# Performance work log

Hardware: AMD Instinct MI355X
Metric: run time of the kernel (lower is better)

The kernel has to match this reference:

```python
import jax, jax.numpy as jnp
import numpy as np

A0 = 0.529177249
SIGMA = jnp.array([0.5515909, 1.8886297, 1.3225029, 1.2316629,
                   2.1884933, 1.7750372, 1.3677907, 1.3820058], dtype=jnp.float32)


def celu(x):
    return jax.nn.celu(x, alpha=0.1)


def setup_inputs() -> dict:
    key = jax.random.key(0)
    ks = jax.random.split(key, 24)
    N, n, L, E = 512, 64, 384, 8
    H1, H2, H3 = 160, 128, 96
    s = 0.05
    f32 = jnp.float32
    return {
        "species": jax.random.randint(ks[0], (N, n), 0, E, dtype=jnp.int32),
        "coordinates": 3.0 * jax.random.normal(ks[1], (N, n, 3), dtype=f32),
        "net_charge": jax.random.normal(ks[2], (N,), dtype=f32),
        "aev": jax.random.normal(ks[3], (N, n, L), dtype=f32),
        "chi_W1": s * jax.random.normal(ks[4], (L, H1), dtype=f32),
        "chi_b1": s * jax.random.normal(ks[5], (H1,), dtype=f32),
        "chi_W2": s * jax.random.normal(ks[6], (H1, H2), dtype=f32),
        "chi_b2": s * jax.random.normal(ks[7], (H2,), dtype=f32),
        "chi_W3": s * jax.random.normal(ks[8], (H2, H3), dtype=f32),
        "chi_b3": s * jax.random.normal(ks[9], (H3,), dtype=f32),
        "chi_W4": s * jax.random.normal(ks[10], (H3, 1), dtype=f32),
        "chi_b4": s * jax.random.normal(ks[11], (1,), dtype=f32),
        "W1": s * jax.random.normal(ks[12], (E, L + 2, H1), dtype=f32),
        "b1": s * jax.random.normal(ks[13], (E, H1), dtype=f32),
        "W2": s * jax.random.normal(ks[14], (E, H1, H2), dtype=f32),
        "b2": s * jax.random.normal(ks[15], (E, H2), dtype=f32),
        "W3": s * jax.random.normal(ks[16], (E, H2, H3), dtype=f32),
        "b3": s * jax.random.normal(ks[17], (E, H3), dtype=f32),
        "W4": s * jax.random.normal(ks[18], (E, H3), dtype=f32),
        "b4": s * jax.random.normal(ks[19], (E,), dtype=f32),
    }


def _forward(species, coordinates, net_charge, aev,
             chi_W1, chi_b1, chi_W2, chi_b2, chi_W3, chi_b3, chi_W4, chi_b4,
             W1, b1, W2, b2, W3, b3, W4, b4):
    N, n = species.shape
    aev_flat = aev.reshape(N * n, -1)                       # (A, L)

    # nonzero_batch_dmat: distances in atomic units, eps avoids div-by-zero
    diff = coordinates[:, None, :, :] - coordinates[:, :, None, :]
    dist = jnp.sqrt(jnp.sum(diff * diff, -1) + 1e-16) / A0   # (N, n, n)

    pad = (species != -1).astype(aev.dtype)                  # (N, n)
    pair_mask = pad[:, None, :] * pad[:, :, None]            # (N, n, n)
    num_atoms = pad.sum(axis=1)                              # (N,)
    valid = (species.reshape(-1) != -1)                      # (A,)

    # chi_net: 4-layer MLP (CELU 0.1) + Softplus, masked to valid atoms
    h = celu(aev_flat @ chi_W1 + chi_b1)
    h = celu(h @ chi_W2 + chi_b2)
    h = celu(h @ chi_W3 + chi_b3)
    chi = jax.nn.softplus(h @ chi_W4 + chi_b4)[:, 0]
    chi = jnp.where(valid, chi, 0.0).reshape(N, n)

    chi_sum = chi.sum(axis=-1)
    k_net = 1.0 + jnp.abs(net_charge) / chi_sum
    chi_mean = chi_sum / num_atoms
    k_p = jnp.where(net_charge > 0, k_net, 1.0)
    k_n = jnp.where(net_charge < 0, k_net, 1.0)
    q = (-k_n[:, None] * chi + (k_p * chi_mean)[:, None]) * pad  # (N, n)

    # ESPerf: pairwise erf-screened Coulomb potential
    sig = SIGMA[jnp.clip(species, 0)]                        # (N, n)
    sig_sqsum = sig[:, None, :] ** 2 + sig[:, :, None] ** 2
    sig_sqsum = jnp.maximum(sig_sqsum, 1e-8)
    j_ij = jax.scipy.special.erf(dist / jnp.sqrt(2.0 * sig_sqsum)) / dist
    diag_mask = 1.0 - jnp.eye(n, dtype=dist.dtype)
    esp = (q[:, :, None] * j_ij * pair_mask * diag_mask[None]).sum(axis=-2)  # (N, n)
    coulomb_energy = 0.5 * (q * esp).sum(axis=-1)            # (N,)

    # species-routed expert MLPs over [aev | charge | esp] features
    feat = jnp.concatenate(
        [aev_flat, q.reshape(-1, 1), esp.reshape(-1, 1)], axis=1)  # (A, L+2)
    h1 = celu(jnp.einsum('ad,edh->aeh', feat, W1) + b1)      # (A, E, H1)
    h2 = celu(jnp.einsum('aeh,ehk->aek', h1, W2) + b2)       # (A, E, H2)
    h3 = celu(jnp.einsum('aek,ekm->aem', h2, W3) + b3)       # (A, E, H3)
    out_all = jnp.einsum('aem,em->ae', h3, W4) + b4          # (A, E)

    sp = jnp.clip(species.reshape(-1), 0)
    out = jnp.take_along_axis(out_all, sp[:, None], axis=1)[:, 0]
    out = jnp.where(valid, out, 0.0).reshape(N, n)
    mol_energy = out.sum(axis=1)
    return species, mol_energy + coulomb_energy, q


def reference(species, coordinates, net_charge, aev,
              chi_W1, chi_b1, chi_W2, chi_b2, chi_W3, chi_b3, chi_W4, chi_b4,
              W1, b1, W2, b2, W3, b3, W4, b4):
    return _forward(species, coordinates, net_charge, aev,
                    chi_W1, chi_b1, chi_W2, chi_b2, chi_W3, chi_b3, chi_W4, chi_b4,
                    W1, b1, W2, b2, W3, b3, W4, b4)
```

## Files before the change

kernel.cpp:

```cpp
#include <hip/hip_runtime.h>
#include <math.h>

#define A0_INV (1.0f/0.529177249f)

typedef __bf16 bf16x8 __attribute__((ext_vector_type(8)));
typedef __bf16 bf16x4 __attribute__((ext_vector_type(4)));
typedef float  f32x4  __attribute__((ext_vector_type(4)));

__device__ __constant__ float c_SIGMA[8] = {
    0.5515909f, 1.8886297f, 1.3225029f, 1.2316629f,
    2.1884933f, 1.7750372f, 1.3677907f, 1.3820058f};

__device__ __forceinline__ float celu01(float x) {
    return x > 0.0f ? x : 0.1f * (__expf(x * 10.0f) - 1.0f);
}
__device__ __forceinline__ float softplusf_(float x) {
    return fmaxf(x, 0.0f) + log1pf(__expf(-fabsf(x)));
}

__device__ __forceinline__ void pack_one(int idx, const float* __restrict__ W,
                                         __bf16* __restrict__ Bp,
                                         int K, int OUT, int NT, int KT)
{
    int lane = idx & 63;
    int rest = idx >> 6;
    int kt = rest % KT; rest /= KT;
    int nt = rest % NT;
    int e  = rest / NT;
    int col = nt * 16 + (lane & 15);
    int k0  = kt * 32 + (lane >> 4) * 8;
    bf16x8 o;
#pragma unroll
    for (int j = 0; j < 8; ++j) {
        int k = k0 + j;
        float v = (k < K) ? W[((long)e * K + k) * OUT + col] : 0.0f;
        o[j] = (__bf16)v;
    }
    *((bf16x8*)Bp + idx) = o;
}

__global__ __launch_bounds__(256) void pack_all_kernel(
    const float* __restrict__ cW1, const float* __restrict__ cW2, const float* __restrict__ cW3,
    const float* __restrict__ W1,  const float* __restrict__ W2,  const float* __restrict__ W3,
    __bf16* bp_c1, __bf16* bp_c2, __bf16* bp_c3,
    __bf16* bp_e1, __bf16* bp_e2, __bf16* bp_e3)
{
    int idx = blockIdx.x * 256 + threadIdx.x;
    if      (idx <   7680) pack_one(idx,          cW1, bp_c1, 384, 160, 10, 12);
    else if (idx <  10240) pack_one(idx - 7680,   cW2, bp_c2, 160, 128,  8,  5);
    else if (idx <  11776) pack_one(idx - 10240,  cW3, bp_c3, 128,  96,  6,  4);
    else if (idx <  78336) pack_one(idx - 11776,  W1,  bp_e1, 386, 160, 10, 13);
    else if (idx <  98816) pack_one(idx - 78336,  W2,  bp_e2, 160, 128,  8,  5);
    else if (idx < 111104) pack_one(idx - 98816,  W3,  bp_e3, 128,  96,  6,  4);
}

template<int NT, int KT, int INS, int OUTS, bool CELU>
__device__ __forceinline__ void mlp_layer8(const __bf16* sIn, const bf16x8* __restrict__ Bp,
                                           const float* __restrict__ bias, __bf16* sOut, int tid)
{
    const int lane = tid & 63;
    const int wid  = tid >> 6;
    const int mw   = wid >> 2;
    const int nw   = wid & 3;
    const int r16  = lane & 15;
    const int g    = lane >> 4;
    constexpr int NJ = (NT + 3) / 4;
    f32x4 acc[2][NJ];
#pragma unroll
    for (int mi = 0; mi < 2; ++mi)
#pragma unroll
        for (int j = 0; j < NJ; ++j)
            acc[mi][j] = (f32x4){0.f, 0.f, 0.f, 0.f};

    bf16x8 bcur[NJ], bnxt[NJ];
#pragma unroll
    for (int j = 0; j < NJ; ++j) {
        const int nt = nw + 4 * j;
        if (nt < NT) bcur[j] = Bp[(nt * KT) * 64 + lane];
    }
    for (int kt = 0; kt < KT; ++kt) {
        bf16x8 a[2];
#pragma unroll
        for (int mi = 0; mi < 2; ++mi)
            a[mi] = *(const bf16x8*)(sIn + ((mw * 2 + mi) * 16 + r16) * INS + kt * 32 + g * 8);
        if (kt + 1 < KT) {
#pragma unroll
            for (int j = 0; j < NJ; ++j) {
                const int nt = nw + 4 * j;
                if (nt < NT) bnxt[j] = Bp[(nt * KT + kt + 1) * 64 + lane];
            }
        }
#pragma unroll
        for (int j = 0; j < NJ; ++j) {
            const int nt = nw + 4 * j;
            if (nt < NT) {
#pragma unroll
                for (int mi = 0; mi < 2; ++mi)
                    acc[mi][j] = __builtin_amdgcn_mfma_f32_16x16x32_bf16(a[mi], bcur[j], acc[mi][j], 0, 0, 0);
            }
        }
#pragma unroll
        for (int j = 0; j < NJ; ++j) bcur[j] = bnxt[j];
    }
#pragma unroll
    for (int j = 0; j < NJ; ++j) {
        const int nt = nw + 4 * j;
        if (nt < NT) {
            const float bb = bias[nt * 16 + r16];
#pragma unroll
            for (int mi = 0; mi < 2; ++mi)
#pragma unroll
                for (int r = 0; r < 4; ++r) {
                    float v = acc[mi][j][r] + bb;
                    if (CELU) v = celu01(v);
                    sOut[((mw * 2 + mi) * 16 + g * 4 + r) * OUTS + nt * 16 + r16] = (__bf16)v;
                }
        }
    }
}

__device__ __forceinline__ float l4_dot(const __bf16* __restrict__ h,
                                        const float* __restrict__ w4)
{
    float acc = 0.f;
#pragma unroll
    for (int u8 = 0; u8 < 12; ++u8) {
        bf16x8 hv = *(const bf16x8*)(h + u8 * 8);
        float4 wa = *(const float4*)(w4 + u8 * 8);
        float4 wb = *(const float4*)(w4 + u8 * 8 + 4);
        acc = fmaf((float)hv[0], wa.x, acc);
        acc = fmaf((float)hv[1], wa.y, acc);
        acc = fmaf((float)hv[2], wa.z, acc);
        acc = fmaf((float)hv[3], wa.w, acc);
        acc = fmaf((float)hv[4], wb.x, acc);
        acc = fmaf((float)hv[5], wb.y, acc);
        acc = fmaf((float)hv[6], wb.z, acc);
        acc = fmaf((float)hv[7], wb.w, acc);
    }
    return acc;
}

__global__ __launch_bounds__(512) void chi_mfma_kernel(
    const float* __restrict__ aev, const int* __restrict__ species,
    const __bf16* __restrict__ bp1, const __bf16* __restrict__ bp2, const __bf16* __restrict__ bp3,
    const float* __restrict__ b1, const float* __restrict__ b2, const float* __restrict__ b3,
    const float* __restrict__ W4, const float* __restrict__ b4,
    float* __restrict__ chi_out, __bf16* __restrict__ aev16,
    int* __restrict__ blockCounts, int* __restrict__ rank)
{
    __shared__ __align__(16) unsigned char smem[50176 + 21504];
    __bf16* sFeat = (__bf16*)smem;
    __bf16* sAct1 = (__bf16*)(smem + 50176);
    __bf16* sAct2 = (__bf16*)smem;
    __bf16* sAct3 = (__bf16*)(smem + 17408);
    const int t = threadIdx.x;
    const long base = (long)blockIdx.x * 64;

    if (aev16) {
        for (int i = t; i < 64 * 96; i += 512) {
            int row = i / 96, c4 = (i - row * 96) * 4;
            float4 v = *(const float4*)(aev + (base + row) * 384 + c4);
            bf16x4 o = {(__bf16)v.x, (__bf16)v.y, (__bf16)v.z, (__bf16)v.w};
            *(bf16x4*)(sFeat + row * 392 + c4) = o;
            *(bf16x4*)(aev16 + (base + row) * 384 + c4) = o;
        }
    } else {
        for (int i = t; i < 64 * 96; i += 512) {
            int row = i / 96, c4 = (i - row * 96) * 4;
            float4 v = *(const float4*)(aev + (base + row) * 384 + c4);
            bf16x4 o = {(__bf16)v.x, (__bf16)v.y, (__bf16)v.z, (__bf16)v.w};
            *(bf16x4*)(sFeat + row * 392 + c4) = o;
        }
    }
    __syncthreads();
    mlp_layer8<10, 12, 392, 168, true>(sFeat, (const bf16x8*)bp1, b1, sAct1, t);
    __syncthreads();
    mlp_layer8<8, 5, 168, 136, true>(sAct1, (const bf16x8*)bp2, b2, sAct2, t);
    __syncthreads();
    mlp_layer8<6, 4, 136, 104, true>(sAct2, (const bf16x8*)bp3, b3, sAct3, t);
    __syncthreads();
    if (t < 64) {
        float acc = l4_dot(sAct3 + t * 104, W4);
        float chiv = softplusf_(acc + b4[0]);
        long atom = base + t;
        int s = species[atom];
        if (s == -1) chiv = 0.f;
        chi_out[atom] = chiv;
        unsigned long long mym = 0;
#pragma unroll
        for (int e = 0; e < 8; ++e) {
            unsigned long long bm = __ballot(s == e);
            if (t == e) blockCounts[blockIdx.x * 8 + e] = (int)__popcll(bm);
            if (s == e) mym = bm;
        }
        if (s >= 0) rank[atom] = (int)__popcll(mym & ((1ull << t) - 1ull));
    }
}

__global__ __launch_bounds__(256) void mol_kernel(
    const int* __restrict__ species, const float* __restrict__ coords,
    const float* __restrict__ netq, const float* __restrict__ chi,
    float* __restrict__ qv, float* __restrict__ esp, float* __restrict__ coul,
    float* __restrict__ o_species, float* __restrict__ o_q)
{
    const int m = blockIdx.x, t = threadIdx.x;
    const int j = t & 63, q4 = t >> 6;
    const int atom = m * 64 + j;
    __shared__ float sx[64], sy[64], sz[64], sq[64], ss2[64];
    __shared__ float sEsp[4][64];

    int s = species[atom];
    float pad = (s != -1) ? 1.0f : 0.0f;
    float chij = chi[atom];

    float cs = chij, na = pad;
#pragma unroll
    for (int o = 32; o > 0; o >>= 1) {
        cs += __shfl_xor(cs, o);
        na += __shfl_xor(na, o);
    }
    float qc = netq[m];
    float k_net = 1.0f + fabsf(qc) / cs;
    float chi_mean = cs / na;
    float k_p = (qc > 0.0f) ? k_net : 1.0f;
    float k_n = (qc < 0.0f) ? k_net : 1.0f;
    float qj = (-k_n * chij + k_p * chi_mean) * pad;

    float sg = c_SIGMA[s < 0 ? 0 : s];
    float x = coords[atom * 3 + 0], y = coords[atom * 3 + 1], z = coords[atom * 3 + 2];
    if (q4 == 0) { sx[j] = x; sy[j] = y; sz[j] = z; sq[j] = qj; ss2[j] = sg * sg; }
    __syncthreads();

    float s2j = sg * sg;
    float ej = 0.0f;
#pragma unroll
    for (int k = 0; k < 16; ++k) {
        int i = q4 * 16 + k;
        if (i == j) continue;
        float dx = sx[i] - x, dy = sy[i] - y, dz = sz[i] - z;
        float d = sqrtf(dx * dx + dy * dy + dz * dz + 1e-16f) * A0_INV;
        float ssum = fmaxf(ss2[i] + s2j, 1e-8f);
        float jij = erff(d * rsqrtf(2.0f * ssum)) / d;
        ej = fmaf(sq[i], jij, ej);
    }
    sEsp[q4][j] = ej;
    __syncthreads();
    if (q4 == 0) {
        float e = (sEsp[0][j] + sEsp[1][j]) + (sEsp[2][j] + sEsp[3][j]);
        e *= pad;
        float ce = qj * e;
#pragma unroll
        for (int o = 32; o > 0; o >>= 1) ce += __shfl_xor(ce, o);
        if (j == 0) coul[m] = 0.5f * ce;
        qv[atom] = qj;
        esp[atom] = e;
        o_species[atom] = (float)s;
        o_q[atom] = qj;
    }
}

__global__ void bucket_scan_kernel(int* __restrict__ blockCounts,
                                   int* __restrict__ counts, int* __restrict__ offs,
                                   int* __restrict__ workItems, int* __restrict__ workCount,
                                   int nb)
{
    __shared__ int segSum[8][8];
    __shared__ int tot[8];
    const int tid = threadIdx.x;
    const int seg = tid >> 3, e = tid & 7;
    const int per = (nb + 7) / 8;
    const int b0 = seg * per, b1 = min(b0 + per, nb);
    int run = 0;
    for (int b = b0; b < b1; ++b) run += blockCounts[b * 8 + e];
    segSum[seg][e] = run;
    __syncthreads();
    if (tid < 8) {
        int r = 0;
        for (int s2 = 0; s2 < 8; ++s2) { int c = segSum[s2][tid]; segSum[s2][tid] = r; r += c; }
        tot[tid] = r;
    }
    __syncthreads();
    int runp = segSum[seg][e];
    for (int b = b0; b < b1; ++b) {
        int c = blockCounts[b * 8 + e];
        blockCounts[b * 8 + e] = runp;
        runp += c;
    }
    if (tid == 0) {
        int o = 0;
        for (int i = 0; i < 8; ++i) { offs[i] = o; counts[i] = tot[i]; o += tot[i]; }
        offs[8] = o;
    }
    if (tid < 8) {
        int pos = 0;
        for (int i = 0; i < tid; ++i) pos += (tot[i] + 63) >> 6;
        int nt_e = (tot[tid] + 63) >> 6;
        for (int k = 0; k < nt_e; ++k) workItems[pos + k] = (tid << 20) | (k * 64);
        if (tid == 7) workCount[0] = pos + nt_e;
    }
}

__global__ __launch_bounds__(256) void bucket_fill_kernel(
    const int* __restrict__ species, const int* __restrict__ blockCounts,
    const int* __restrict__ offs, const int* __restrict__ rank,
    int* __restrict__ bidx, float* __restrict__ outat, int A)
{
    int a = blockIdx.x * 256 + threadIdx.x;
    if (a < A) {
        outat[a] = 0.0f;
        int s = species[a];
        if (s >= 0)
            bidx[offs[s] + blockCounts[(a >> 6) * 8 + s] + rank[a]] = a;
    }
}

__global__ __launch_bounds__(512) void expert_mfma_kernel(
    const float* __restrict__ aev, const __bf16* __restrict__ aev16,
    const float* __restrict__ qv, const float* __restrict__ esp,
    const __bf16* __restrict__ bp1, const __bf16* __restrict__ bp2, const __bf16* __restrict__ bp3,
    const float* __restrict__ b1, const float* __restrict__ b2, const float* __restrict__ b3,
    const float* __restrict__ W4, const float* __restrict__ b4,
    const int* __restrict__ counts, const int* __restrict__ offs, const int* __restrict__ bidx,
    const int* __restrict__ workItems, const int* __restrict__ workCount,
    float* __restrict__ outat)
{
    const int bid = blockIdx.x;
    if (bid >= workCount[0]) return;
    const int wi = workItems[bid];
    const int e = wi >> 20;
    const int start = wi & 0xFFFFF;
    const int cnt = counts[e];

    __shared__ __align__(16) unsigned char smem[54272 + 21504];
    __shared__ int said[64];
    __bf16* sFeat = (__bf16*)smem;
    __bf16* sAct1 = (__bf16*)(smem + 54272);
    __bf16* sAct2 = (__bf16*)smem;
    __bf16* sAct3 = (__bf16*)(smem + 17408);
    const int t = threadIdx.x;

    if (t < 64) said[t] = (start + t < cnt) ? bidx[offs[e] + start + t] : -1;
    __syncthreads();

    if (aev16) {
        for (int i = t; i < 64 * 48; i += 512) {
            int row = i / 48, c = (i - row * 48) * 8;
            int atom = said[row];
            bf16x8 v = {(__bf16)0.f, (__bf16)0.f, (__bf16)0.f, (__bf16)0.f,
                        (__bf16)0.f, (__bf16)0.f, (__bf16)0.f, (__bf16)0.f};
            if (atom >= 0) v = *(const bf16x8*)(aev16 + (long)atom * 384 + c);
            *(bf16x8*)(sFeat + row * 424 + c) = v;
        }
    } else {
        for (int i = t; i < 64 * 96; i += 512) {
            int row = i / 96, c4 = (i - row * 96) * 4;
            int atom = said[row];
            bf16x4 o = {(__bf16)0.f, (__bf16)0.f, (__bf16)0.f, (__bf16)0.f};
            if (atom >= 0) {
                float4 v = *(const float4*)(aev + (long)atom * 384 + c4);
                o[0] = (__bf16)v.x; o[1] = (__bf16)v.y;
                o[2] = (__bf16)v.z; o[3] = (__bf16)v.w;
            }
            *(bf16x4*)(sFeat + row * 424 + c4) = o;
        }
    }
    if (t < 64) {
        int atom = said[t];
        float a0 = 0.f, a1 = 0.f;
        if (atom >= 0) { a0 = qv[atom]; a1 = esp[atom]; }
        sFeat[t * 424 + 384] = (__bf16)a0;
        sFeat[t * 424 + 385] = (__bf16)a1;
        for (int c = 386; c < 416; ++c) sFeat[t * 424 + c] = (__bf16)0.f;
    }
    __syncthreads();
    mlp_layer8<10, 13, 424, 168, true>(sFeat, (const bf16x8*)bp1 + (size_t)e * 10 * 13 * 64,
                                       b1 + e * 160, sAct1, t);
    __syncthreads();
    mlp_layer8<8, 5, 168, 136, true>(sAct1, (const bf16x8*)bp2 + (size_t)e * 8 * 5 * 64,
                                     b2 + e * 128, sAct2, t);
    __syncthreads();
    mlp_layer8<6, 4, 136, 104, true>(sAct2, (const bf16x8*)bp3 + (size_t)e * 6 * 4 * 64,
                                     b3 + e * 96, sAct3, t);
    __syncthreads();
    if (t < 64) {
        int atom = said[t];
        if (atom >= 0) {
            float acc = l4_dot(sAct3 + t * 104, W4 + e * 96);
            outat[atom] = acc + b4[e];
        }
    }
}

__global__ __launch_bounds__(64) void energy_kernel(
    const float* __restrict__ outat, const float* __restrict__ coul,
    float* __restrict__ o_energy)
{
    int m = blockIdx.x, t = threadIdx.x;
    float v = outat[m * 64 + t];
#pragma unroll
    for (int o = 32; o > 0; o >>= 1) v += __shfl_xor(v, o);
    if (t == 0) o_energy[m] = v + coul[m];
}

extern "C" void kernel_launch(void* const* d_in, const int* in_sizes, int n_in,
                              void* d_out, int out_size, void* d_ws, size_t ws_size,
                              hipStream_t stream)
{
    const int*   species = (const int*)  d_in[0];
    const float* coords  = (const float*)d_in[1];
    const float* netq    = (const float*)d_in[2];
    const float* aev     = (const float*)d_in[3];
    const float* cW1 = (const float*)d_in[4];
    const float* cb1 = (const float*)d_in[5];
    const float* cW2 = (const float*)d_in[6];
    const float* cb2 = (const float*)d_in[7];
    const float* cW3 = (const float*)d_in[8];
    const float* cb3 = (const float*)d_in[9];
    const float* cW4 = (const float*)d_in[10];
    const float* cb4 = (const float*)d_in[11];
    const float* W1  = (const float*)d_in[12];
    const float* b1  = (const float*)d_in[13];
    const float* W2  = (const float*)d_in[14];
    const float* b2  = (const float*)d_in[15];
    const float* W3  = (const float*)d_in[16];
    const float* b3  = (const float*)d_in[17];
    const float* W4  = (const float*)d_in[18];
    const float* b4  = (const float*)d_in[19];

    const int N = in_sizes[2];
    const int n = in_sizes[0] / N;
    const int A = N * n;
    const int nb64 = A / 64;
    const int maxWork = nb64 + 8;

    float* fbase   = (float*)d_ws;
    float* chi     = fbase;
    float* qv      = fbase + (size_t)A;
    float* esp     = fbase + (size_t)2 * A;
    float* outat   = fbase + (size_t)3 * A;
    float* coul    = fbase + (size_t)4 * A;
    int*   counts  = (int*)(coul + N);
    int*   offs    = counts + 8;
    int*   workCount = offs + 9;
    int*   workItems = workCount + 1;
    int*   blockCounts = workItems + maxWork;
    int*   rank    = blockCounts + nb64 * 8;
    int*   bidx    = rank + A;
    uintptr_t p = ((uintptr_t)(bidx + A) + 15) & ~(uintptr_t)15;
    __bf16* bp_c1 = (__bf16*)p; p += (size_t)10 * 12 * 512 * 2;
    __bf16* bp_c2 = (__bf16*)p; p += (size_t)8  * 5  * 512 * 2;
    __bf16* bp_c3 = (__bf16*)p; p += (size_t)6  * 4  * 512 * 2;
    __bf16* bp_e1 = (__bf16*)p; p += (size_t)8 * 10 * 13 * 512 * 2;
    __bf16* bp_e2 = (__bf16*)p; p += (size_t)8 * 8  * 5  * 512 * 2;
    __bf16* bp_e3 = (__bf16*)p; p += (size_t)8 * 6  * 4  * 512 * 2;
    p = (p + 15) & ~(uintptr_t)15;
    __bf16* aev16 = (__bf16*)p;
    size_t need = (p - (uintptr_t)d_ws) + (size_t)A * 384 * 2;
    if (ws_size < need) aev16 = nullptr;

    float* o_species = (float*)d_out;
    float* o_energy  = o_species + A;
    float* o_q       = o_energy + N;

    pack_all_kernel<<<(111104 + 255) / 256, 256, 0, stream>>>(
        cW1, cW2, cW3, W1, W2, W3, bp_c1, bp_c2, bp_c3, bp_e1, bp_e2, bp_e3);

    chi_mfma_kernel<<<nb64, 512, 0, stream>>>(aev, species, bp_c1, bp_c2, bp_c3,
                                              cb1, cb2, cb3, cW4, cb4, chi,
                                              aev16, blockCounts, rank);
    mol_kernel<<<N, 256, 0, stream>>>(species, coords, netq, chi, qv, esp, coul,
                                      (float*)d_out, o_q);
    bucket_scan_kernel<<<1, 64, 0, stream>>>(blockCounts, counts, offs,
                                             workItems, workCount, nb64);
    bucket_fill_kernel<<<(A + 255) / 256, 256, 0, stream>>>(species, blockCounts, offs,
                                                            rank, bidx, outat, A);
    expert_mfma_kernel<<<maxWork, 512, 0, stream>>>(aev, aev16, qv, esp,
                                                    bp_e1, bp_e2, bp_e3,
                                                    b1, b2, b3, W4, b4,
                                                    counts, offs, bidx,
                                                    workItems, workCount, outat);
    energy_kernel<<<N, 64, 0, stream>>>(outat, coul, o_energy);
}
```

Before: 91.56 us.

## Fuse chi MLP with molecule charge kernel; stream expert layer-1 A from global

Merges the chi MLP kernel and the per-molecule charge/ESP kernel into one launch, since each 64-atom block is exactly one molecule. Chi then stays in shared memory and one kernel launch plus a global round trip go away. The expert kernel's first layer now loads the gathered AEV rows straight from global into registers with software prefetch instead of staging them in shared memory. This shrinks LDS use and raises the occupancy hint to 6 blocks. The extra q/esp features are packed into a final MFMA step, and the bf16/f32 source choice becomes a template parameter.

```diff
diff --git a/kernel.cpp b/kernel.cpp
--- a/kernel.cpp
+++ b/kernel.cpp
@@ -16,6 +16,12 @@
 }
 __device__ __forceinline__ float softplusf_(float x) {
     return fmaxf(x, 0.0f) + log1pf(__expf(-fabsf(x)));
+}
+__device__ __forceinline__ __bf16 u16_to_bf16(unsigned short u) {
+    __bf16 b; __builtin_memcpy(&b, &u, 2); return b;
+}
+__device__ __forceinline__ unsigned short f_to_bf16_bits(float f) {
+    __bf16 b = (__bf16)f; unsigned short u; __builtin_memcpy(&u, &b, 2); return u;
 }
 
 __device__ __forceinline__ void pack_one(int idx, const float* __restrict__ W,
@@ -140,21 +146,28 @@
     return acc;
 }
 
-__global__ __launch_bounds__(512) void chi_mfma_kernel(
+__global__ __launch_bounds__(512) void chimol_kernel(
     const float* __restrict__ aev, const int* __restrict__ species,
+    const float* __restrict__ coords, const float* __restrict__ netq,
     const __bf16* __restrict__ bp1, const __bf16* __restrict__ bp2, const __bf16* __restrict__ bp3,
     const float* __restrict__ b1, const float* __restrict__ b2, const float* __restrict__ b3,
     const float* __restrict__ W4, const float* __restrict__ b4,
-    float* __restrict__ chi_out, __bf16* __restrict__ aev16,
-    int* __restrict__ blockCounts, int* __restrict__ rank)
+    __bf16* __restrict__ aev16,
+    int* __restrict__ blockCounts, int* __restrict__ rank,
+    float* __restrict__ qv, float* __restrict__ esp, float* __restrict__ coul,
+    float* __restrict__ o_species, float* __restrict__ o_q)
 {
     __shared__ __align__(16) unsigned char smem[50176 + 21504];
+    __shared__ float sChi[64];
+    __shared__ float sx[64], sy[64], sz[64], sq[64], ss2[64];
+    __shared__ float sEsp[8][64];
     __bf16* sFeat = (__bf16*)smem;
     __bf16* sAct1 = (__bf16*)(smem + 50176);
     __bf16* sAct2 = (__bf16*)smem;
     __bf16* sAct3 = (__bf16*)(smem + 17408);
     const int t = threadIdx.x;
-    const long base = (long)blockIdx.x * 64;
+    const int m = blockIdx.x;
+    const long base = (long)m * 64;
 
     if (aev16) {
         for (int i = t; i < 64 * 96; i += 512) {
@@ -185,33 +198,23 @@
         long atom = base + t;
         int s = species[atom];
         if (s == -1) chiv = 0.f;
-        chi_out[atom] = chiv;
+        sChi[t] = chiv;
         unsigned long long mym = 0;
 #pragma unroll
         for (int e = 0; e < 8; ++e) {
             unsigned long long bm = __ballot(s == e);
-            if (t == e) blockCounts[blockIdx.x * 8 + e] = (int)__popcll(bm);
+            if (t == e) blockCounts[m * 8 + e] = (int)__popcll(bm);
             if (s == e) mym = bm;
         }
         if (s >= 0) rank[atom] = (int)__popcll(mym & ((1ull << t) - 1ull));
     }
-}
-
-__global__ __launch_bounds__(256) void mol_kernel(
-    const int* __restrict__ species, const float* __restrict__ coords,
-    const float* __restrict__ netq, const float* __restrict__ chi,
-    float* __restrict__ qv, float* __restrict__ esp, float* __restrict__ coul,
-    float* __restrict__ o_species, float* __restrict__ o_q)
-{
-    const int m = blockIdx.x, t = threadIdx.x;
-    const int j = t & 63, q4 = t >> 6;
-    const int atom = m * 64 + j;
-    __shared__ float sx[64], sy[64], sz[64], sq[64], ss2[64];
-    __shared__ float sEsp[4][64];
-
+    __syncthreads();
+
+    const int j = t & 63, grp = t >> 6;
+    const int atom = (int)base + j;
     int s = species[atom];
     float pad = (s != -1) ? 1.0f : 0.0f;
-    float chij = chi[atom];
+    float chij = sChi[j];
 
     float cs = chij, na = pad;
 #pragma unroll
@@ -228,14 +231,14 @@
 
     float sg = c_SIGMA[s < 0 ? 0 : s];
     float x = coords[atom * 3 + 0], y = coords[atom * 3 + 1], z = coords[atom * 3 + 2];
-    if (q4 == 0) { sx[j] = x; sy[j] = y; sz[j] = z; sq[j] = qj; ss2[j] = sg * sg; }
+    if (grp == 0) { sx[j] = x; sy[j] = y; sz[j] = z; sq[j] = qj; ss2[j] = sg * sg; }
     __syncthreads();
 
     float s2j = sg * sg;
     float ej = 0.0f;
 #pragma unroll
-    for (int k = 0; k < 16; ++k) {
-        int i = q4 * 16 + k;
+    for (int k = 0; k < 8; ++k) {
+        int i = grp * 8 + k;
         if (i == j) continue;
         float dx = sx[i] - x, dy = sy[i] - y, dz = sz[i] - z;
         float d = sqrtf(dx * dx + dy * dy + dz * dz + 1e-16f) * A0_INV;
@@ -243,10 +246,11 @@
         float jij = erff(d * rsqrtf(2.0f * ssum)) / d;
         ej = fmaf(sq[i], jij, ej);
     }
-    sEsp[q4][j] = ej;
-    __syncthreads();
-    if (q4 == 0) {
-        float e = (sEsp[0][j] + sEsp[1][j]) + (sEsp[2][j] + sEsp[3][j]);
+    sEsp[grp][j] = ej;
+    __syncthreads();
+    if (grp == 0) {
+        float e = ((sEsp[0][j] + sEsp[1][j]) + (sEsp[2][j] + sEsp[3][j]))
+                + ((sEsp[4][j] + sEsp[5][j]) + (sEsp[6][j] + sEsp[7][j]));
         e *= pad;
         float ce = qj * e;
 #pragma unroll
@@ -314,7 +318,27 @@
     }
 }
 
-__global__ __launch_bounds__(512) void expert_mfma_kernel(
+__device__ __forceinline__ bf16x8 loadA16(const __bf16* __restrict__ aev16,
+                                          int atom, int kt, int g)
+{
+    bf16x8 z = {};
+    if (atom < 0) return z;
+    return *(const bf16x8*)(aev16 + (long)atom * 384 + kt * 32 + g * 8);
+}
+__device__ __forceinline__ bf16x8 loadAf(const float* __restrict__ aev,
+                                         int atom, int kt, int g)
+{
+    bf16x8 z = {};
+    if (atom < 0) return z;
+    const float* p = aev + (long)atom * 384 + kt * 32 + g * 8;
+    float4 va = *(const float4*)p, vb = *(const float4*)(p + 4);
+    bf16x8 r = {(__bf16)va.x, (__bf16)va.y, (__bf16)va.z, (__bf16)va.w,
+                (__bf16)vb.x, (__bf16)vb.y, (__bf16)vb.z, (__bf16)vb.w};
+    return r;
+}
+
+template<bool HAVE16>
+__global__ __launch_bounds__(512, 6) void expert_mfma_kernel(
     const float* __restrict__ aev, const __bf16* __restrict__ aev16,
     const float* __restrict__ qv, const float* __restrict__ esp,
     const __bf16* __restrict__ bp1, const __bf16* __restrict__ bp2, const __bf16* __restrict__ bp3,
@@ -331,50 +355,102 @@
     const int start = wi & 0xFFFFF;
     const int cnt = counts[e];
 
-    __shared__ __align__(16) unsigned char smem[54272 + 21504];
+    __shared__ __align__(16) unsigned char smem[21504 + 17408];
     __shared__ int said[64];
-    __bf16* sFeat = (__bf16*)smem;
-    __bf16* sAct1 = (__bf16*)(smem + 54272);
-    __bf16* sAct2 = (__bf16*)smem;
-    __bf16* sAct3 = (__bf16*)(smem + 17408);
+    __shared__ unsigned int sQE[64];
+    __bf16* sAct1 = (__bf16*)smem;
+    __bf16* sAct2 = (__bf16*)(smem + 21504);
+    __bf16* sAct3 = (__bf16*)smem;
     const int t = threadIdx.x;
 
-    if (t < 64) said[t] = (start + t < cnt) ? bidx[offs[e] + start + t] : -1;
-    __syncthreads();
-
-    if (aev16) {
-        for (int i = t; i < 64 * 48; i += 512) {
-            int row = i / 48, c = (i - row * 48) * 8;
-            int atom = said[row];
-            bf16x8 v = {(__bf16)0.f, (__bf16)0.f, (__bf16)0.f, (__bf16)0.f,
-                        (__bf16)0.f, (__bf16)0.f, (__bf16)0.f, (__bf16)0.f};
-            if (atom >= 0) v = *(const bf16x8*)(aev16 + (long)atom * 384 + c);
-            *(bf16x8*)(sFeat + row * 424 + c) = v;
-        }
-    } else {
-        for (int i = t; i < 64 * 96; i += 512) {
-            int row = i / 96, c4 = (i - row * 96) * 4;
-            int atom = said[row];
-            bf16x4 o = {(__bf16)0.f, (__bf16)0.f, (__bf16)0.f, (__bf16)0.f};
-            if (atom >= 0) {
-                float4 v = *(const float4*)(aev + (long)atom * 384 + c4);
-                o[0] = (__bf16)v.x; o[1] = (__bf16)v.y;
-                o[2] = (__bf16)v.z; o[3] = (__bf16)v.w;
-            }
-            *(bf16x4*)(sFeat + row * 424 + c4) = o;
-        }
-    }
     if (t < 64) {
-        int atom = said[t];
-        float a0 = 0.f, a1 = 0.f;
-        if (atom >= 0) { a0 = qv[atom]; a1 = esp[atom]; }
-        sFeat[t * 424 + 384] = (__bf16)a0;
-        sFeat[t * 424 + 385] = (__bf16)a1;
-        for (int c = 386; c < 416; ++c) sFeat[t * 424 + c] = (__bf16)0.f;
-    }
-    __syncthreads();
-    mlp_layer8<10, 13, 424, 168, true>(sFeat, (const bf16x8*)bp1 + (size_t)e * 10 * 13 * 64,
-                                       b1 + e * 160, sAct1, t);
+        int a_ = (start + t < cnt) ? bidx[offs[e] + start + t] : -1;
+        said[t] = a_;
+        float q = 0.f, es = 0.f;
+        if (a_ >= 0) { q = qv[a_]; es = esp[a_]; }
+        sQE[t] = ((unsigned)f_to_bf16_bits(es) << 16) | f_to_bf16_bits(q);
+    }
+    __syncthreads();
+
+    {
+        const int lane = t & 63, wid = t >> 6;
+        const int mw = wid >> 2, nw = wid & 3;
+        const int r16 = lane & 15, g = lane >> 4;
+        const int atom0 = said[(mw * 2 + 0) * 16 + r16];
+        const int atom1 = said[(mw * 2 + 1) * 16 + r16];
+        const bf16x8* Bp = (const bf16x8*)bp1 + (size_t)e * 10 * 13 * 64;
+        constexpr int NJ = 3;
+        f32x4 acc[2][NJ];
+#pragma unroll
+        for (int mi = 0; mi < 2; ++mi)
+#pragma unroll
+            for (int j = 0; j < NJ; ++j) acc[mi][j] = (f32x4){0.f, 0.f, 0.f, 0.f};
+
+        bf16x8 bcur[NJ], bnxt[NJ];
+#pragma unroll
+        for (int j = 0; j < NJ; ++j) {
+            const int nt = nw + 4 * j;
+            if (nt < 10) bcur[j] = Bp[(nt * 13) * 64 + lane];
+        }
+        bf16x8 a0c = HAVE16 ? loadA16(aev16, atom0, 0, g) : loadAf(aev, atom0, 0, g);
+        bf16x8 a1c = HAVE16 ? loadA16(aev16, atom1, 0, g) : loadAf(aev, atom1, 0, g);
+
+        for (int kt = 0; kt < 12; ++kt) {
+#pragma unroll
+            for (int j = 0; j < NJ; ++j) {
+                const int nt = nw + 4 * j;
+                if (nt < 10) bnxt[j] = Bp[(nt * 13 + kt + 1) * 64 + lane];
+            }
+            bf16x8 a0n, a1n;
+            if (kt < 11) {
+                a0n = HAVE16 ? loadA16(aev16, atom0, kt + 1, g) : loadAf(aev, atom0, kt + 1, g);
+                a1n = HAVE16 ? loadA16(aev16, atom1, kt + 1, g) : loadAf(aev, atom1, kt + 1, g);
+            }
+#pragma unroll
+            for (int j = 0; j < NJ; ++j) {
+                const int nt = nw + 4 * j;
+                if (nt < 10) {
+                    acc[0][j] = __builtin_amdgcn_mfma_f32_16x16x32_bf16(a0c, bcur[j], acc[0][j], 0, 0, 0);
+                    acc[1][j] = __builtin_amdgcn_mfma_f32_16x16x32_bf16(a1c, bcur[j], acc[1][j], 0, 0, 0);
+                }
+            }
+#pragma unroll
+            for (int j = 0; j < NJ; ++j) bcur[j] = bnxt[j];
+            if (kt < 11) { a0c = a0n; a1c = a1n; }
+        }
+        bf16x8 aq0 = {}, aq1 = {};
+        if (g == 0) {
+            unsigned qe0 = sQE[(mw * 2 + 0) * 16 + r16];
+            unsigned qe1 = sQE[(mw * 2 + 1) * 16 + r16];
+            aq0[0] = u16_to_bf16((unsigned short)(qe0 & 0xffff));
+            aq0[1] = u16_to_bf16((unsigned short)(qe0 >> 16));
+            aq1[0] = u16_to_bf16((unsigned short)(qe1 & 0xffff));
+            aq1[1] = u16_to_bf16((unsigned short)(qe1 >> 16));
+        }
+#pragma unroll
+        for (int j = 0; j < NJ; ++j) {
+            const int nt = nw + 4 * j;
+            if (nt < 10) {
+                acc[0][j] = __builtin_amdgcn_mfma_f32_16x16x32_bf16(aq0, bcur[j], acc[0][j], 0, 0, 0);
+                acc[1][j] = __builtin_amdgcn_mfma_f32_16x16x32_bf16(aq1, bcur[j], acc[1][j], 0, 0, 0);
+            }
+        }
+#pragma unroll
+        for (int j = 0; j < NJ; ++j) {
+            const int nt = nw + 4 * j;
+            if (nt < 10) {
+                const float bb = b1[e * 160 + nt * 16 + r16];
+#pragma unroll
+                for (int mi = 0; mi < 2; ++mi)
+#pragma unroll
+                    for (int r = 0; r < 4; ++r) {
+                        float v = acc[mi][j][r] + bb;
+                        v = celu01(v);
+                        sAct1[((mw * 2 + mi) * 16 + g * 4 + r) * 168 + nt * 16 + r16] = (__bf16)v;
+                    }
+            }
+        }
+    }
     __syncthreads();
     mlp_layer8<8, 5, 168, 136, true>(sAct1, (const bf16x8*)bp2 + (size_t)e * 8 * 5 * 64,
                                      b2 + e * 128, sAct2, t);
@@ -434,11 +510,10 @@
     const int maxWork = nb64 + 8;
 
     float* fbase   = (float*)d_ws;
-    float* chi     = fbase;
-    float* qv      = fbase + (size_t)A;
-    float* esp     = fbase + (size_t)2 * A;
-    float* outat   = fbase + (size_t)3 * A;
-    float* coul    = fbase + (size_t)4 * A;
+    float* qv      = fbase;
+    float* esp     = fbase + (size_t)A;
+    float* outat   = fbase + (size_t)2 * A;
+    float* coul    = fbase + (size_t)3 * A;
     int*   counts  = (int*)(coul + N);
     int*   offs    = counts + 8;
     int*   workCount = offs + 9;
@@ -465,19 +540,22 @@
     pack_all_kernel<<<(111104 + 255) / 256, 256, 0, stream>>>(
         cW1, cW2, cW3, W1, W2, W3, bp_c1, bp_c2, bp_c3, bp_e1, bp_e2, bp_e3);
 
-    chi_mfma_kernel<<<nb64, 512, 0, stream>>>(aev, species, bp_c1, bp_c2, bp_c3,
-                                              cb1, cb2, cb3, cW4, cb4, chi,
-                                              aev16, blockCounts, rank);
-    mol_kernel<<<N, 256, 0, stream>>>(species, coords, netq, chi, qv, esp, coul,
-                                      (float*)d_out, o_q);
+    chimol_kernel<<<nb64, 512, 0, stream>>>(aev, species, coords, netq,
+                                            bp_c1, bp_c2, bp_c3,
+                                            cb1, cb2, cb3, cW4, cb4,
+                                            aev16, blockCounts, rank,
+                                            qv, esp, coul, o_species, o_q);
     bucket_scan_kernel<<<1, 64, 0, stream>>>(blockCounts, counts, offs,
                                              workItems, workCount, nb64);
     bucket_fill_kernel<<<(A + 255) / 256, 256, 0, stream>>>(species, blockCounts, offs,
                                                             rank, bidx, outat, A);
-    expert_mfma_kernel<<<maxWork, 512, 0, stream>>>(aev, aev16, qv, esp,
-                                                    bp_e1, bp_e2, bp_e3,
-                                                    b1, b2, b3, W4, b4,
-                                                    counts, offs, bidx,
-                                                    workItems, workCount, outat);
+    if (aev16)
+        expert_mfma_kernel<true><<<maxWork, 512, 0, stream>>>(
+            aev, aev16, qv, esp, bp_e1, bp_e2, bp_e3, b1, b2, b3, W4, b4,
+            counts, offs, bidx, workItems, workCount, outat);
+    else
+        expert_mfma_kernel<false><<<maxWork, 512, 0, stream>>>(
+            aev, aev16, qv, esp, bp_e1, bp_e2, bp_e3, b1, b2, b3, W4, b4,
+            counts, offs, bidx, workItems, workCount, outat);
     energy_kernel<<<N, 64, 0, stream>>>(outat, coul, o_energy);
 }
```

New measurement: 113.4 us. +23.8%, slower.
